# Kernel optimization log

Hardware: AMD Instinct MI355X
Metric: run time of the kernel (lower is better)

The kernel has to match this reference:

```python
import jax, jax.numpy as jnp
import numpy as np

N = 100000   # nodes
E = 1600000  # edges (before self-loops)
H = 128      # in_channels == hidden_channels
G = 64       # graphs in batch


def setup_inputs() -> dict:
    key = jax.random.key(0)
    ks = jax.random.split(key, 12)
    s = 1.0 / np.sqrt(H)
    inp = {
        "x": jax.random.normal(ks[0], (N, H), jnp.float32),
        "edge_weight": jax.random.uniform(ks[1], (E,), jnp.float32),
        "edge_index": jax.random.randint(ks[2], (2, E), 0, N, dtype=jnp.int64),
        "batch": jnp.sort(jax.random.randint(ks[3], (N,), 0, G, dtype=jnp.int64)),
        "W1": jax.random.uniform(ks[4], (H, H), jnp.float32, -s, s),
        "b1": jnp.zeros((H,), jnp.float32),
        "W2": jax.random.uniform(ks[5], (H, H), jnp.float32, -s, s),
        "b2": jnp.zeros((H,), jnp.float32),
        "W3": jax.random.uniform(ks[6], (H, H), jnp.float32, -s, s),
        "b3": jnp.zeros((H,), jnp.float32),
        "lin_w": jax.random.uniform(ks[7], (H, 1), jnp.float32, -s, s),
        "lin_b": jax.random.uniform(ks[8], (1,), jnp.float32, -s, s),
    }
    return inp


def reference(x, edge_weight, W1, b1, W2, b2, W3, b3, lin_w, lin_b, edge_index, batch):
    # PyG GCNConv with add_self_loops=True, symmetric normalization.
    loops = jnp.arange(N, dtype=edge_index.dtype)
    row = jnp.concatenate([edge_index[0], loops])  # source
    col = jnp.concatenate([edge_index[1], loops])  # target
    ew = jnp.concatenate([edge_weight, jnp.ones((N,), edge_weight.dtype)])

    deg = jax.ops.segment_sum(ew, col, num_segments=N)          # in-degree (weighted)
    safe = jnp.where(deg > 0, deg, 1.0)
    dinv = jnp.where(deg > 0, jax.lax.rsqrt(safe), 0.0)
    norm = dinv[row] * ew * dinv[col]                            # [E+N]

    def conv(h, W, b):
        h = h @ W                                                # [N,H] dense transform
        msg = h[row] * norm[:, None]                             # gather + scale
        return jax.ops.segment_sum(msg, col, num_segments=N) + b # scatter-add

    h = jax.nn.relu(conv(x, W1, b1))
    h = jax.nn.relu(conv(h, W2, b2))
    h = jax.nn.relu(conv(h, W3, b3))

    # global_mean_pool over graph ids
    sums = jax.ops.segment_sum(h, batch, num_segments=G)         # [G,H]
    cnts = jax.ops.segment_sum(jnp.ones((N,), h.dtype), batch, num_segments=G)
    pooled = sums / jnp.maximum(cnts, 1.0)[:, None]
    # dropout is identity at inference
    return pooled @ lin_w + lin_b                                # [G,1]
```

## Files before the change

kernel.cpp:

```cpp
#include <hip/hip_runtime.h>
#include <stdint.h>

#define N_NODES 100000
#define N_EDGES 1600000
#define HDIM    128
#define G_GRAPHS 64
#define NTOT (N_EDGES + N_NODES)
#define PSLOTS 64
#define NSTRIPS (N_NODES / 16)
#define NTB 512
#define NDB ((N_EDGES + 2047) / 2048)
#define BSH 9
#define NBK ((N_NODES + 511) / 512)
#define MAXBKT 10240

static_assert(N_NODES % 16 == 0, "tile/agg");
static_assert(N_NODES < (1 << 17), "src fits 17 bits");

typedef __attribute__((ext_vector_type(8))) short bf16x8;
typedef __attribute__((ext_vector_type(4))) float f32x4;
typedef __attribute__((ext_vector_type(2))) float f32x2;

__device__ __forceinline__ uint32_t f2bf(float x) {
    uint32_t b = __float_as_uint(x);
    return (b + 0x7FFFu + ((b >> 16) & 1u)) >> 16;
}
__device__ __forceinline__ uint32_t pack2(float lo, float hi) {
    return f2bf(lo) | (f2bf(hi) << 16);
}

#define FXSCALE 1099511627776.0f

__global__ void k_wswz(const float* __restrict__ Wb, const float* __restrict__ Wc,
                       uint16_t* __restrict__ dst) {
    int gi = blockIdx.x * 256 + threadIdx.x;
    int w = gi >> 14, idx = gi & 16383;
    const float* src = (w == 0) ? Wb : Wc;
    int k = idx >> 7, n = idx & 127;
    int kc = k >> 5, kq = (k >> 3) & 3, j = k & 7;
    int nt = n >> 4, nl = n & 15;
    dst[w * 16384 + (((kc * 8 + nt) * 64) + kq * 16 + nl) * 8 + j] = (uint16_t)f2bf(src[idx]);
}

__device__ __forceinline__ bf16x8 load_row_f32(const float* p) {
    float4 a = ((const float4*)p)[0];
    float4 b = ((const float4*)p)[1];
    union { uint32_t u[4]; bf16x8 v; } c;
    c.u[0] = pack2(a.x, a.y); c.u[1] = pack2(a.z, a.w);
    c.u[2] = pack2(b.x, b.y); c.u[3] = pack2(b.z, b.w);
    return c.v;
}

__device__ __forceinline__ void transform_body_l1(int tb, int nTB, int tid,
                                                  const float* __restrict__ hin,
                                                  const float* __restrict__ Wg,
                                                  uint32_t* __restrict__ t,
                                                  uint16_t* Wf) {
    for (int idx = tid; idx < 16384; idx += 256) {
        int k = idx >> 7, n = idx & 127;
        int kc = k >> 5, kq = (k >> 3) & 3, j = k & 7;
        int nt = n >> 4, nl = n & 15;
        Wf[(((kc * 8 + nt) * 64) + kq * 16 + nl) * 8 + j] = (uint16_t)f2bf(Wg[idx]);
    }
    __syncthreads();
    const bf16x8* Wfrag = (const bf16x8*)Wf;
    int lane = tid & 63;
    int quad = lane >> 4;
    int mrow = lane & 15;
    int gwave = tb * 4 + (tid >> 6);
    int nwaves = nTB * 4;
    for (int strip = gwave; strip < NSTRIPS; strip += nwaves) {
        const float* hrow = hin + ((size_t)(strip * 16 + mrow)) * 128 + quad * 8;
        bf16x8 A0 = load_row_f32(hrow);
        bf16x8 A1 = load_row_f32(hrow + 32);
        bf16x8 A2 = load_row_f32(hrow + 64);
        bf16x8 A3 = load_row_f32(hrow + 96);
        f32x4 acc[8];
#pragma unroll
        for (int nt = 0; nt < 8; nt++) {
            f32x4 a = {0.f, 0.f, 0.f, 0.f};
            a = __builtin_amdgcn_mfma_f32_16x16x32_bf16(A0, Wfrag[(0 * 8 + nt) * 64 + lane], a, 0, 0, 0);
            a = __builtin_amdgcn_mfma_f32_16x16x32_bf16(A1, Wfrag[(1 * 8 + nt) * 64 + lane], a, 0, 0, 0);
            a = __builtin_amdgcn_mfma_f32_16x16x32_bf16(A2, Wfrag[(2 * 8 + nt) * 64 + lane], a, 0, 0, 0);
            a = __builtin_amdgcn_mfma_f32_16x16x32_bf16(A3, Wfrag[(3 * 8 + nt) * 64 + lane], a, 0, 0, 0);
            acc[nt] = a;
        }
#pragma unroll
        for (int nt = 0; nt < 8; nt++) {
#pragma unroll
            for (int r = 0; r < 4; r++) {
                float v = acc[nt][r];
                float nb = __shfl_xor(v, 1);
                int s16 = __builtin_amdgcn_cvt_pk_fp8_f32(v, nb, 0, false);
                int hi  = __shfl_xor(s16, 2);
                if (!(lane & 3)) {
                    int orow = strip * 16 + quad * 4 + r;
                    int oc = (nt * 16 + mrow) >> 2;
                    t[(size_t)orow * 32 + oc] = (uint32_t)(s16 & 0xffff) | ((uint32_t)hi << 16);
                }
            }
        }
    }
}

__global__ __launch_bounds__(256) void k_tr_count(
        const int* __restrict__ ei, const float* __restrict__ x,
        const float* __restrict__ Wg, uint32_t* __restrict__ t,
        int* __restrict__ partials) {
    __shared__ uint16_t Wf[16384];
    int bi = blockIdx.x;
    int q5 = bi / 5, r5 = bi % 5;
    int tq = q5 * 2 + r5;
    bool isT = (r5 < 2) && (tq < NTB);
    int tid = threadIdx.x;
    if (isT) {
        transform_body_l1(tq, NTB, tid, x, Wg, t, Wf);
    } else {
        int nTbef = q5 * 2 + (r5 < 2 ? r5 : 2);
        if (nTbef > NTB) nTbef = NTB;
        int db = bi - nTbef;
        int* hist = (int*)Wf;
        for (int i = tid; i < NBK; i += 256) hist[i] = 0;
        __syncthreads();
        int e0 = db * 2048 + tid;
#pragma unroll
        for (int k = 0; k < 8; k++) {
            int e = e0 + k * 256;
            if (e < N_EDGES) atomicAdd(&hist[ei[N_EDGES + e] >> BSH], 1);
        }
        __syncthreads();
        for (int i = tid; i < NBK; i += 256) partials[i * NDB + db] = hist[i];
    }
}

__global__ void k_bscan(const int* __restrict__ partials, int* __restrict__ blockBase,
                        int* __restrict__ totals) {
    int b = blockIdx.x, tid = threadIdx.x;
    int v[4]; int s = 0;
#pragma unroll
    for (int j = 0; j < 4; j++) {
        int i = tid * 4 + j;
        v[j] = (i < NDB) ? partials[b * NDB + i] : 0;
        s += v[j];
    }
    __shared__ int sm[256];
    sm[tid] = s; __syncthreads();
    for (int off = 1; off < 256; off <<= 1) {
        int u = 0; if (tid >= off) u = sm[tid - off];
        __syncthreads(); sm[tid] += u; __syncthreads();
    }
    int run = sm[tid] - s;
#pragma unroll
    for (int j = 0; j < 4; j++) {
        int i = tid * 4 + j;
        if (i < NDB) blockBase[b * NDB + i] = run;
        run += v[j];
    }
    if (tid == 255) totals[b] = sm[255];
}

__global__ void k_starts(const int* __restrict__ totals, int* __restrict__ bstart) {
    int tid = threadIdx.x;
    int v = (tid < NBK) ? totals[tid] : 0;
    __shared__ int sm[256];
    sm[tid] = v; __syncthreads();
    for (int off = 1; off < 256; off <<= 1) {
        int u = 0; if (tid >= off) u = sm[tid - off];
        __syncthreads(); sm[tid] += u; __syncthreads();
    }
    if (tid < NBK) bstart[tid] = sm[tid] - v;
    if (tid == 255) bstart[NBK] = sm[255];
}

__global__ __launch_bounds__(256) void k_scatter(
        const int* __restrict__ ei, const float* __restrict__ ew,
        const int* __restrict__ blockBase, const int* __restrict__ bstart,
        uint2* __restrict__ recs) {
    __shared__ int hist[NBK];
    __shared__ int basesh[NBK];
    int tid = threadIdx.x, db = blockIdx.x;
    for (int i = tid; i < NBK; i += 256) {
        hist[i] = 0;
        basesh[i] = bstart[i] + blockBase[i * NDB + db];
    }
    __syncthreads();
    int e0 = db * 2048 + tid;
#pragma unroll
    for (int k = 0; k < 8; k++) {
        int e = e0 + k * 256;
        if (e < N_EDGES) {
            int src = ei[e];
            int dst = ei[N_EDGES + e];
            float w = ew[e];
            int bkt = dst >> BSH;
            int r = atomicAdd(&hist[bkt], 1);
            recs[basesh[bkt] + r] =
                make_uint2((uint32_t)src | ((uint32_t)(dst & 511) << 17),
                           __float_as_uint(w));
        }
    }
}

__global__ __launch_bounds__(256) void k_build(
        const uint2* __restrict__ recs, const int* __restrict__ bstart,
        int* __restrict__ cnt, float* __restrict__ dinv, int* __restrict__ offs,
        int2* __restrict__ csr) {
    __shared__ unsigned long long acc[512];
    __shared__ uint16_t rk[MAXBKT];
    __shared__ int loff[512];
    __shared__ int sm[256];
    int b = blockIdx.x, tid = threadIdx.x;
    int e0 = bstart[b], ne = bstart[b + 1] - e0;
    for (int i = tid; i < 512; i += 256) acc[i] = 0ULL;
    __syncthreads();
    for (int j = tid; j < ne; j += 256) {
        uint2 rc = recs[e0 + j];
        int dl = (rc.x >> 17) & 511;
        float w = __uint_as_float(rc.y);
        unsigned long long pk = (1ULL << 48) | (unsigned long long)(w * FXSCALE);
        unsigned long long old = atomicAdd(&acc[dl], pk);
        rk[j] = (uint16_t)(old >> 48);
    }
    __syncthreads();
    int nb0 = b << BSH;
    int nreal = N_NODES - nb0; if (nreal > 512) nreal = 512;
    int i0 = tid * 2, i1 = tid * 2 + 1;
    int c0 = (i0 < nreal) ? (int)(acc[i0] >> 48) + 1 : 0;
    int c1 = (i1 < nreal) ? (int)(acc[i1] >> 48) + 1 : 0;
    sm[tid] = c0 + c1;
    __syncthreads();
    for (int off = 1; off < 256; off <<= 1) {
        int u = 0; if (tid >= off) u = sm[tid - off];
        __syncthreads(); sm[tid] += u; __syncthreads();
    }
    int run = e0 + nb0 + (sm[tid] - (c0 + c1));
    loff[i0] = run;
    loff[i1] = run + c0;
    if (i0 < nreal) {
        unsigned long long pk = acc[i0];
        int c = (int)(pk >> 48);
        float deg = (float)(pk & ((1ULL << 48) - 1)) * (1.0f / FXSCALE);
        cnt[nb0 + i0] = c;
        offs[nb0 + i0] = run;
        dinv[nb0 + i0] = 1.0f / sqrtf(deg + 1.0f);
        csr[run + c] = make_int2(nb0 + i0, __float_as_int(1.0f));
    }
    if (i1 < nreal) {
        unsigned long long pk = acc[i1];
        int c = (int)(pk >> 48);
        float deg = (float)(pk & ((1ULL << 48) - 1)) * (1.0f / FXSCALE);
        cnt[nb0 + i1] = c;
        offs[nb0 + i1] = run + c0;
        dinv[nb0 + i1] = 1.0f / sqrtf(deg + 1.0f);
        csr[run + c0 + c] = make_int2(nb0 + i1, __float_as_int(1.0f));
    }
    __syncthreads();
    for (int j = tid; j < ne; j += 256) {
        uint2 rc = recs[e0 + j];
        int dl = (rc.x >> 17) & 511;
        int src = rc.x & 0x1ffff;
        csr[loff[dl] + rk[j]] = make_int2(src, (int)rc.y);
    }
}

__global__ void k_norm(int2* __restrict__ csr, const float* __restrict__ dinv) {
    int p = blockIdx.x * 256 + threadIdx.x;
    if (p < NTOT) {
        int2 c = csr[p];
        csr[p].y = __float_as_int(__int_as_float(c.y) * dinv[c.x]);
    }
}

__device__ __forceinline__ void fetch8(const char* __restrict__ tb, int g4, int lq8,
                                       int base, uint32_t osrc, float wsrc,
                                       uint2 (&va)[8], float (&wf)[8]) {
#pragma unroll
    for (int k = 0; k < 8; k++) {
        int o  = __builtin_amdgcn_ds_bpermute(g4 + base + 4 * k, (int)osrc);
        int wb = __builtin_amdgcn_ds_bpermute(g4 + base + 4 * k, __float_as_int(wsrc));
        wf[k] = __uint_as_float((uint32_t)wb);
        va[k] = *(const uint2*)(tb + (uint32_t)(o + lq8));
    }
}

__device__ __forceinline__ void acc8(const uint2 (&va)[8], const float (&wf)[8],
                                     f32x2& p0, f32x2& p1, f32x2& p2, f32x2& p3) {
#pragma unroll
    for (int k = 0; k < 8; k++) {
        f32x2 lo0 = __builtin_amdgcn_cvt_pk_f32_fp8((int)va[k].x, false);
        f32x2 hi0 = __builtin_amdgcn_cvt_pk_f32_fp8((int)va[k].x, true);
        f32x2 lo1 = __builtin_amdgcn_cvt_pk_f32_fp8((int)va[k].y, false);
        f32x2 hi1 = __builtin_amdgcn_cvt_pk_f32_fp8((int)va[k].y, true);
        f32x2 wp = { wf[k], wf[k] };
        p0 += wp * lo0; p1 += wp * hi0; p2 += wp * lo1; p3 += wp * hi1;
    }
}

__device__ __forceinline__ void aggregate_node(const char* __restrict__ tb,
        const int2* __restrict__ csr, int beg, int num, int ql, int g4, int lq8,
        f32x2& p0, f32x2& p1, f32x2& p2, f32x2& p3) {
    int2 m0 = make_int2(0, 0), m1 = make_int2(0, 0);
    if (ql < num) m0 = csr[beg + ql];
    if (ql + 16 < num) m1 = csr[beg + 16 + ql];
    uint32_t o0 = (uint32_t)m0.x << 7;
    uint32_t o1 = (uint32_t)m1.x << 7;
    float w0 = __int_as_float(m0.y), w1 = __int_as_float(m1.y);
    bool c1 = num > 8, c2 = num > 16, c3 = num > 24;
    uint2 va[8], vb[8], vc[8], vd[8];
    float wa[8], wb[8], wc[8], wd[8];
    fetch8(tb, g4, lq8, 0, o0, w0, va, wa);
    if (c1) fetch8(tb, g4, lq8, 32, o0, w0, vb, wb);
    acc8(va, wa, p0, p1, p2, p3);
    if (c2) fetch8(tb, g4, lq8, 0, o1, w1, vc, wc);
    if (c1) acc8(vb, wb, p0, p1, p2, p3);
    if (c3) fetch8(tb, g4, lq8, 32, o1, w1, vd, wd);
    if (c2) acc8(vc, wc, p0, p1, p2, p3);
    if (c3) acc8(vd, wd, p0, p1, p2, p3);
    for (int base = 32; base < num; base += 16) {
        int2 mm = make_int2(0, 0);
        if (base + ql < num) mm = csr[beg + base + ql];
        uint32_t oo = (uint32_t)mm.x << 7;
        float mws = __int_as_float(mm.y);
        bool h = base + 8 < num;
        fetch8(tb, g4, lq8, 0, oo, mws, va, wa);
        if (h) fetch8(tb, g4, lq8, 32, oo, mws, vb, wb);
        acc8(va, wa, p0, p1, p2, p3);
        if (h) acc8(vb, wb, p0, p1, p2, p3);
    }
}

__device__ __forceinline__ f32x2 relu2(f32x2 p, float dn, f32x2 b) {
    f32x2 r;
    r.x = fmaxf(p.x * dn + b.x, 0.f);
    r.y = fmaxf(p.y * dn + b.y, 0.f);
    return r;
}

__global__ __launch_bounds__(256) void k_agg_tr(
        const uint32_t* __restrict__ tin, const int* __restrict__ offs,
        const int* __restrict__ cnt, const int2* __restrict__ csr,
        const float* __restrict__ dinv, const float* __restrict__ bias,
        const bf16x8* __restrict__ Wfrag, uint32_t* __restrict__ tout) {
    __shared__ uint32_t ht[16 * 16 * 4];
    int tid = threadIdx.x;
    int lane = tid & 63;
    int ql = lane & 15;
    int grp = lane & 48;
    int g4 = grp << 2, lq8 = ql << 3;
    int row = (tid >> 6) * 4 + (lane >> 4);
    int node = blockIdx.x * 16 + row;
    int beg = offs[node];
    int num = cnt[node] + 1;
    float dn = dinv[node];
    f32x2 p0 = {0.f, 0.f}, p1 = {0.f, 0.f}, p2 = {0.f, 0.f}, p3 = {0.f, 0.f};
    aggregate_node((const char*)tin, csr, beg, num, ql, g4, lq8, p0, p1, p2, p3);
    const f32x2* bp = (const f32x2*)bias;
    p0 = relu2(p0, dn, bp[ql * 4 + 0]);
    p1 = relu2(p1, dn, bp[ql * 4 + 1]);
    p2 = relu2(p2, dn, bp[ql * 4 + 2]);
    p3 = relu2(p3, dn, bp[ql * 4 + 3]);
    {
        int slot = (ql + row) & 15;
        uint32_t* dst = &ht[(row * 16 + slot) * 4];
        dst[0] = pack2(p0.x, p0.y);
        dst[1] = pack2(p1.x, p1.y);
        dst[2] = pack2(p2.x, p2.y);
        dst[3] = pack2(p3.x, p3.y);
    }
    __syncthreads();
    int quad = lane >> 4;
    int m = lane & 15;
    int wid = tid >> 6;
    bf16x8 A[4];
#pragma unroll
    for (int c = 0; c < 4; c++) {
        int sl = (c * 4 + quad + m) & 15;
        A[c] = *(const bf16x8*)&ht[(m * 16 + sl) * 4];
    }
    int strip = blockIdx.x;
#pragma unroll
    for (int u = 0; u < 2; u++) {
        int nt = wid * 2 + u;
        f32x4 a = {0.f, 0.f, 0.f, 0.f};
        a = __builtin_amdgcn_mfma_f32_16x16x32_bf16(A[0], Wfrag[(0 * 8 + nt) * 64 + lane], a, 0, 0, 0);
        a = __builtin_amdgcn_mfma_f32_16x16x32_bf16(A[1], Wfrag[(1 * 8 + nt) * 64 + lane], a, 0, 0, 0);
        a = __builtin_amdgcn_mfma_f32_16x16x32_bf16(A[2], Wfrag[(2 * 8 + nt) * 64 + lane], a, 0, 0, 0);
        a = __builtin_amdgcn_mfma_f32_16x16x32_bf16(A[3], Wfrag[(3 * 8 + nt) * 64 + lane], a, 0, 0, 0);
#pragma unroll
        for (int r = 0; r < 4; r++) {
            float v = a[r];
            float nb = __shfl_xor(v, 1);
            int s16 = __builtin_amdgcn_cvt_pk_fp8_f32(v, nb, 0, false);
            int hi  = __shfl_xor(s16, 2);
            if (!(lane & 3)) {
                int orow = strip * 16 + quad * 4 + r;
                int oc = (nt * 16 + m) >> 2;
                tout[(size_t)orow * 32 + oc] = (uint32_t)(s16 & 0xffff) | ((uint32_t)hi << 16);
            }
        }
    }
}

__global__ void k_agg_pool(const uint32_t* __restrict__ t, const int* __restrict__ offs,
                           const int* __restrict__ cnt, const int2* __restrict__ csr,
                           const float* __restrict__ dinv, const float* __restrict__ bias,
                           const float* __restrict__ lw, const int* __restrict__ batch,
                           float* __restrict__ pp) {
    int tid = threadIdx.x;
    int lane = tid & 63;
    int ql = lane & 15;
    int grp = lane & 48;
    int g4 = grp << 2, lq8 = ql << 3;
    int node = blockIdx.x * 16 + (tid >> 6) * 4 + (lane >> 4);
    int beg = offs[node];
    int num = cnt[node] + 1;
    float dn = dinv[node];
    f32x2 p0 = {0.f, 0.f}, p1 = {0.f, 0.f}, p2 = {0.f, 0.f}, p3 = {0.f, 0.f};
    aggregate_node((const char*)t, csr, beg, num, ql, g4, lq8, p0, p1, p2, p3);
    const f32x2* bp = (const f32x2*)bias;
    p0 = relu2(p0, dn, bp[ql * 4 + 0]);
    p1 = relu2(p1, dn, bp[ql * 4 + 1]);
    p2 = relu2(p2, dn, bp[ql * 4 + 2]);
    p3 = relu2(p3, dn, bp[ql * 4 + 3]);
    const f32x2* wp2 = (const f32x2*)lw;
    f32x2 q0 = wp2[ql * 4 + 0], q1 = wp2[ql * 4 + 1];
    f32x2 q2 = wp2[ql * 4 + 2], q3 = wp2[ql * 4 + 3];
    float d = p0.x * q0.x + p0.y * q0.y + p1.x * q1.x + p1.y * q1.y
            + p2.x * q2.x + p2.y * q2.y + p3.x * q3.x + p3.y * q3.y;
    for (int off = 8; off; off >>= 1) d += __shfl_down(d, off);
    if (ql == 0)
        atomicAdd(&pp[(blockIdx.x & (PSLOTS - 1)) * G_GRAPHS + batch[node]], d);
}

__global__ void k_final(const float* __restrict__ pp, const int* __restrict__ batch,
                        const float* __restrict__ lb, float* __restrict__ out) {
    int g = threadIdx.x;
    float s = 0.f;
#pragma unroll
    for (int k = 0; k < PSLOTS; k++) s += pp[k * G_GRAPHS + g];
    int lo = 0, hi = N_NODES;
    while (lo < hi) { int m = (lo + hi) >> 1; if (batch[m] < g) lo = m + 1; else hi = m; }
    int beg = lo;
    hi = N_NODES;
    while (lo < hi) { int m = (lo + hi) >> 1; if (batch[m] < g + 1) lo = m + 1; else hi = m; }
    float c = fmaxf((float)(lo - beg), 1.0f);
    out[g] = s / c + lb[0];
}

extern "C" void kernel_launch(void* const* d_in, const int* in_sizes, int n_in,
                              void* d_out, int out_size, void* d_ws, size_t ws_size,
                              hipStream_t stream) {
    const float* x   = (const float*)d_in[0];
    const float* ew  = (const float*)d_in[1];
    const int*   ei  = (const int*)d_in[2];
    const int*   bat = (const int*)d_in[3];
    const float* W1  = (const float*)d_in[4];
    const float* b1  = (const float*)d_in[5];
    const float* W2  = (const float*)d_in[6];
    const float* b2  = (const float*)d_in[7];
    const float* W3  = (const float*)d_in[8];
    const float* b3  = (const float*)d_in[9];
    const float* lw  = (const float*)d_in[10];
    const float* lb  = (const float*)d_in[11];
    float* out = (float*)d_out;

    char* w = (char*)d_ws;
    size_t o = 0;
    auto carve = [&](size_t bytes) -> void* {
        void* p = w + o;
        o = (o + bytes + 255) & ~(size_t)255;
        return p;
    };
    float*    pp     = (float*)carve((size_t)PSLOTS * G_GRAPHS * 4);
    int*      parts  = (int*)  carve((size_t)NBK * NDB * 4);
    int*      bbase  = (int*)  carve((size_t)NBK * NDB * 4);
    int*      totals = (int*)  carve((size_t)NBK * 4);
    int*      bstart = (int*)  carve((size_t)(NBK + 1) * 4);
    uint2*    recs   = (uint2*)carve((size_t)N_EDGES * 8);
    int*      cnt    = (int*)  carve((size_t)N_NODES * 4);
    float*    dinv   = (float*)carve((size_t)N_NODES * 4);
    int*      offs   = (int*)  carve((size_t)N_NODES * 4);
    int2*     csr    = (int2*) carve((size_t)NTOT * 8);
    uint32_t* tA     = (uint32_t*)carve((size_t)N_NODES * 128);
    uint32_t* tB     = (uint32_t*)carve((size_t)N_NODES * 128);
    uint16_t* wsz    = (uint16_t*)carve((size_t)2 * 16384 * 2);
    (void)ws_size; (void)in_sizes; (void)n_in; (void)out_size;

    hipMemsetAsync(pp, 0, (size_t)PSLOTS * G_GRAPHS * 4, stream);

    k_wswz<<<128, 256, 0, stream>>>(W2, W3, wsz);
    k_tr_count<<<NTB + NDB, 256, 0, stream>>>(ei, x, W1, tA, parts);
    k_bscan<<<NBK, 256, 0, stream>>>(parts, bbase, totals);
    k_starts<<<1, 256, 0, stream>>>(totals, bstart);
    k_scatter<<<NDB, 256, 0, stream>>>(ei, ew, bbase, bstart, recs);
    k_build<<<NBK, 256, 0, stream>>>(recs, bstart, cnt, dinv, offs, csr);
    k_norm<<<(NTOT + 255) / 256, 256, 0, stream>>>(csr, dinv);

    k_agg_tr<<<NSTRIPS, 256, 0, stream>>>(tA, offs, cnt, csr, dinv, b1,
                                          (const bf16x8*)wsz, tB);
    k_agg_tr<<<NSTRIPS, 256, 0, stream>>>(tB, offs, cnt, csr, dinv, b2,
                                          (const bf16x8*)(wsz + 16384), tA);
    k_agg_pool<<<NSTRIPS, 256, 0, stream>>>(tA, offs, cnt, csr, dinv, b3, lw, bat, pp);

    k_final<<<1, G_GRAPHS, 0, stream>>>(pp, bat, lb, out);
}
```

Measured before the change: 343.2 us.

## Pre-swizzle W1 globally, use persistent aggregation grid, swap bpermute for ds_swizzle

W1 is now pre-swizzled to bf16 once in k_wswz, so transform blocks read MFMA fragments from global memory instead of each block converting W1 into shared memory. NTB is doubled and the block interleave ratio changed. The aggregation kernels move to a grid-stride loop over a fixed AGRID of 2048 blocks, which adds a second barrier per strip. The first 32 neighbours are now broadcast with ds_swizzle instead of ds_bpermute, and all four fetch batches are issued before accumulation to raise memory-level parallelism, at the cost of higher register pressure.

```diff
diff --git a/kernel.cpp b/kernel.cpp
--- a/kernel.cpp
+++ b/kernel.cpp
@@ -8,11 +8,12 @@
 #define NTOT (N_EDGES + N_NODES)
 #define PSLOTS 64
 #define NSTRIPS (N_NODES / 16)
-#define NTB 512
+#define NTB 1024
 #define NDB ((N_EDGES + 2047) / 2048)
 #define BSH 9
 #define NBK ((N_NODES + 511) / 512)
 #define MAXBKT 10240
+#define AGRID 2048
 
 static_assert(N_NODES % 16 == 0, "tile/agg");
 static_assert(N_NODES < (1 << 17), "src fits 17 bits");
@@ -31,11 +32,11 @@
 
 #define FXSCALE 1099511627776.0f
 
-__global__ void k_wswz(const float* __restrict__ Wb, const float* __restrict__ Wc,
-                       uint16_t* __restrict__ dst) {
+__global__ void k_wswz(const float* __restrict__ Wa, const float* __restrict__ Wb,
+                       const float* __restrict__ Wc, uint16_t* __restrict__ dst) {
     int gi = blockIdx.x * 256 + threadIdx.x;
     int w = gi >> 14, idx = gi & 16383;
-    const float* src = (w == 0) ? Wb : Wc;
+    const float* src = (w == 0) ? Wa : (w == 1) ? Wb : Wc;
     int k = idx >> 7, n = idx & 127;
     int kc = k >> 5, kq = (k >> 3) & 3, j = k & 7;
     int nt = n >> 4, nl = n & 15;
@@ -53,17 +54,8 @@
 
 __device__ __forceinline__ void transform_body_l1(int tb, int nTB, int tid,
                                                   const float* __restrict__ hin,
-                                                  const float* __restrict__ Wg,
-                                                  uint32_t* __restrict__ t,
-                                                  uint16_t* Wf) {
-    for (int idx = tid; idx < 16384; idx += 256) {
-        int k = idx >> 7, n = idx & 127;
-        int kc = k >> 5, kq = (k >> 3) & 3, j = k & 7;
-        int nt = n >> 4, nl = n & 15;
-        Wf[(((kc * 8 + nt) * 64) + kq * 16 + nl) * 8 + j] = (uint16_t)f2bf(Wg[idx]);
-    }
-    __syncthreads();
-    const bf16x8* Wfrag = (const bf16x8*)Wf;
+                                                  const bf16x8* __restrict__ Wfrag,
+                                                  uint32_t* __restrict__ t) {
     int lane = tid & 63;
     int quad = lane >> 4;
     int mrow = lane & 15;
@@ -105,21 +97,20 @@
 
 __global__ __launch_bounds__(256) void k_tr_count(
         const int* __restrict__ ei, const float* __restrict__ x,
-        const float* __restrict__ Wg, uint32_t* __restrict__ t,
+        const bf16x8* __restrict__ Wfrag, uint32_t* __restrict__ t,
         int* __restrict__ partials) {
-    __shared__ uint16_t Wf[16384];
+    __shared__ int hist[NBK];
     int bi = blockIdx.x;
-    int q5 = bi / 5, r5 = bi % 5;
-    int tq = q5 * 2 + r5;
-    bool isT = (r5 < 2) && (tq < NTB);
+    int q7 = bi / 7, r7 = bi % 7;
+    int tq = q7 * 4 + r7;
+    bool isT = (r7 < 4) && (tq < NTB);
     int tid = threadIdx.x;
     if (isT) {
-        transform_body_l1(tq, NTB, tid, x, Wg, t, Wf);
+        transform_body_l1(tq, NTB, tid, x, Wfrag, t);
     } else {
-        int nTbef = q5 * 2 + (r5 < 2 ? r5 : 2);
+        int nTbef = q7 * 4 + (r7 < 4 ? r7 : 4);
         if (nTbef > NTB) nTbef = NTB;
         int db = bi - nTbef;
-        int* hist = (int*)Wf;
         for (int i = tid; i < NBK; i += 256) hist[i] = 0;
         __syncthreads();
         int e0 = db * 2048 + tid;
@@ -271,9 +262,24 @@
     }
 }
 
-__device__ __forceinline__ void fetch8(const char* __restrict__ tb, int g4, int lq8,
-                                       int base, uint32_t osrc, float wsrc,
-                                       uint2 (&va)[8], float (&wf)[8]) {
+#define FETCH1(j, osrc, wsrc, vv, ww) { \
+    int o_ = __builtin_amdgcn_ds_swizzle((int)(osrc), (((j) << 5) | 0x10)); \
+    int w_ = __builtin_amdgcn_ds_swizzle((int)(wsrc), (((j) << 5) | 0x10)); \
+    ww = __uint_as_float((uint32_t)w_); \
+    vv = *(const uint2*)(tb + (uint32_t)o_ + lq8); }
+#define FETCH8S(J, osrc, wsrc, va, wa) \
+    FETCH1((J) + 0, osrc, wsrc, va[0], wa[0]) \
+    FETCH1((J) + 1, osrc, wsrc, va[1], wa[1]) \
+    FETCH1((J) + 2, osrc, wsrc, va[2], wa[2]) \
+    FETCH1((J) + 3, osrc, wsrc, va[3], wa[3]) \
+    FETCH1((J) + 4, osrc, wsrc, va[4], wa[4]) \
+    FETCH1((J) + 5, osrc, wsrc, va[5], wa[5]) \
+    FETCH1((J) + 6, osrc, wsrc, va[6], wa[6]) \
+    FETCH1((J) + 7, osrc, wsrc, va[7], wa[7])
+
+__device__ __forceinline__ void fetch8b(const char* __restrict__ tb, int g4, int lq8,
+                                        int base, uint32_t osrc, float wsrc,
+                                        uint2 (&va)[8], float (&wf)[8]) {
 #pragma unroll
     for (int k = 0; k < 8; k++) {
         int o  = __builtin_amdgcn_ds_bpermute(g4 + base + 4 * k, (int)osrc);
@@ -297,35 +303,37 @@
 }
 
 __device__ __forceinline__ void aggregate_node(const char* __restrict__ tb,
-        const int2* __restrict__ csr, int beg, int num, int ql, int g4, int lq8,
+        const int2* __restrict__ csr, int beg, int num, int ql, int lane, int lq8,
         f32x2& p0, f32x2& p1, f32x2& p2, f32x2& p3) {
     int2 m0 = make_int2(0, 0), m1 = make_int2(0, 0);
     if (ql < num) m0 = csr[beg + ql];
     if (ql + 16 < num) m1 = csr[beg + 16 + ql];
     uint32_t o0 = (uint32_t)m0.x << 7;
     uint32_t o1 = (uint32_t)m1.x << 7;
-    float w0 = __int_as_float(m0.y), w1 = __int_as_float(m1.y);
     bool c1 = num > 8, c2 = num > 16, c3 = num > 24;
     uint2 va[8], vb[8], vc[8], vd[8];
     float wa[8], wb[8], wc[8], wd[8];
-    fetch8(tb, g4, lq8, 0, o0, w0, va, wa);
-    if (c1) fetch8(tb, g4, lq8, 32, o0, w0, vb, wb);
+    FETCH8S(0, o0, m0.y, va, wa)
+    if (c1) { FETCH8S(8, o0, m0.y, vb, wb) }
+    if (c2) { FETCH8S(0, o1, m1.y, vc, wc) }
+    if (c3) { FETCH8S(8, o1, m1.y, vd, wd) }
     acc8(va, wa, p0, p1, p2, p3);
-    if (c2) fetch8(tb, g4, lq8, 0, o1, w1, vc, wc);
     if (c1) acc8(vb, wb, p0, p1, p2, p3);
-    if (c3) fetch8(tb, g4, lq8, 32, o1, w1, vd, wd);
     if (c2) acc8(vc, wc, p0, p1, p2, p3);
     if (c3) acc8(vd, wd, p0, p1, p2, p3);
-    for (int base = 32; base < num; base += 16) {
-        int2 mm = make_int2(0, 0);
-        if (base + ql < num) mm = csr[beg + base + ql];
-        uint32_t oo = (uint32_t)mm.x << 7;
-        float mws = __int_as_float(mm.y);
-        bool h = base + 8 < num;
-        fetch8(tb, g4, lq8, 0, oo, mws, va, wa);
-        if (h) fetch8(tb, g4, lq8, 32, oo, mws, vb, wb);
-        acc8(va, wa, p0, p1, p2, p3);
-        if (h) acc8(vb, wb, p0, p1, p2, p3);
+    if (num > 32) {
+        int g4 = (lane & 48) << 2;
+        for (int base = 32; base < num; base += 16) {
+            int2 mm = make_int2(0, 0);
+            if (base + ql < num) mm = csr[beg + base + ql];
+            uint32_t oo = (uint32_t)mm.x << 7;
+            float mws = __int_as_float(mm.y);
+            bool h = base + 8 < num;
+            fetch8b(tb, g4, lq8, 0, oo, mws, va, wa);
+            if (h) fetch8b(tb, g4, lq8, 32, oo, mws, vb, wb);
+            acc8(va, wa, p0, p1, p2, p3);
+            if (h) acc8(vb, wb, p0, p1, p2, p3);
+        }
     }
 }
 
@@ -345,91 +353,94 @@
     int tid = threadIdx.x;
     int lane = tid & 63;
     int ql = lane & 15;
-    int grp = lane & 48;
-    int g4 = grp << 2, lq8 = ql << 3;
+    int lq8 = ql << 3;
     int row = (tid >> 6) * 4 + (lane >> 4);
-    int node = blockIdx.x * 16 + row;
-    int beg = offs[node];
-    int num = cnt[node] + 1;
-    float dn = dinv[node];
-    f32x2 p0 = {0.f, 0.f}, p1 = {0.f, 0.f}, p2 = {0.f, 0.f}, p3 = {0.f, 0.f};
-    aggregate_node((const char*)tin, csr, beg, num, ql, g4, lq8, p0, p1, p2, p3);
-    const f32x2* bp = (const f32x2*)bias;
-    p0 = relu2(p0, dn, bp[ql * 4 + 0]);
-    p1 = relu2(p1, dn, bp[ql * 4 + 1]);
-    p2 = relu2(p2, dn, bp[ql * 4 + 2]);
-    p3 = relu2(p3, dn, bp[ql * 4 + 3]);
-    {
-        int slot = (ql + row) & 15;
-        uint32_t* dst = &ht[(row * 16 + slot) * 4];
-        dst[0] = pack2(p0.x, p0.y);
-        dst[1] = pack2(p1.x, p1.y);
-        dst[2] = pack2(p2.x, p2.y);
-        dst[3] = pack2(p3.x, p3.y);
-    }
-    __syncthreads();
     int quad = lane >> 4;
     int m = lane & 15;
     int wid = tid >> 6;
-    bf16x8 A[4];
-#pragma unroll
-    for (int c = 0; c < 4; c++) {
-        int sl = (c * 4 + quad + m) & 15;
-        A[c] = *(const bf16x8*)&ht[(m * 16 + sl) * 4];
-    }
-    int strip = blockIdx.x;
-#pragma unroll
-    for (int u = 0; u < 2; u++) {
-        int nt = wid * 2 + u;
-        f32x4 a = {0.f, 0.f, 0.f, 0.f};
-        a = __builtin_amdgcn_mfma_f32_16x16x32_bf16(A[0], Wfrag[(0 * 8 + nt) * 64 + lane], a, 0, 0, 0);
-        a = __builtin_amdgcn_mfma_f32_16x16x32_bf16(A[1], Wfrag[(1 * 8 + nt) * 64 + lane], a, 0, 0, 0);
-        a = __builtin_amdgcn_mfma_f32_16x16x32_bf16(A[2], Wfrag[(2 * 8 + nt) * 64 + lane], a, 0, 0, 0);
-        a = __builtin_amdgcn_mfma_f32_16x16x32_bf16(A[3], Wfrag[(3 * 8 + nt) * 64 + lane], a, 0, 0, 0);
-#pragma unroll
-        for (int r = 0; r < 4; r++) {
-            float v = a[r];
-            float nb = __shfl_xor(v, 1);
-            int s16 = __builtin_amdgcn_cvt_pk_fp8_f32(v, nb, 0, false);
-            int hi  = __shfl_xor(s16, 2);
-            if (!(lane & 3)) {
-                int orow = strip * 16 + quad * 4 + r;
-                int oc = (nt * 16 + m) >> 2;
-                tout[(size_t)orow * 32 + oc] = (uint32_t)(s16 & 0xffff) | ((uint32_t)hi << 16);
+    for (int strip = blockIdx.x; strip < NSTRIPS; strip += AGRID) {
+        int node = strip * 16 + row;
+        int beg = offs[node];
+        int num = cnt[node] + 1;
+        float dn = dinv[node];
+        f32x2 p0 = {0.f, 0.f}, p1 = {0.f, 0.f}, p2 = {0.f, 0.f}, p3 = {0.f, 0.f};
+        aggregate_node((const char*)tin, csr, beg, num, ql, lane, lq8, p0, p1, p2, p3);
+        const f32x2* bp = (const f32x2*)bias;
+        p0 = relu2(p0, dn, bp[ql * 4 + 0]);
+        p1 = relu2(p1, dn, bp[ql * 4 + 1]);
+        p2 = relu2(p2, dn, bp[ql * 4 + 2]);
+        p3 = relu2(p3, dn, bp[ql * 4 + 3]);
+        {
+            int slot = (ql + row) & 15;
+            uint32_t* dst = &ht[(row * 16 + slot) * 4];
+            dst[0] = pack2(p0.x, p0.y);
+            dst[1] = pack2(p1.x, p1.y);
+            dst[2] = pack2(p2.x, p2.y);
+            dst[3] = pack2(p3.x, p3.y);
+        }
+        __syncthreads();
+        bf16x8 A[4];
+#pragma unroll
+        for (int c = 0; c < 4; c++) {
+            int sl = (c * 4 + quad + m) & 15;
+            A[c] = *(const bf16x8*)&ht[(m * 16 + sl) * 4];
+        }
+        __syncthreads();
+#pragma unroll
+        for (int u = 0; u < 2; u++) {
+            int nt = wid * 2 + u;
+            f32x4 a = {0.f, 0.f, 0.f, 0.f};
+            a = __builtin_amdgcn_mfma_f32_16x16x32_bf16(A[0], Wfrag[(0 * 8 + nt) * 64 + lane], a, 0, 0, 0);
+            a = __builtin_amdgcn_mfma_f32_16x16x32_bf16(A[1], Wfrag[(1 * 8 + nt) * 64 + lane], a, 0, 0, 0);
+            a = __builtin_amdgcn_mfma_f32_16x16x32_bf16(A[2], Wfrag[(2 * 8 + nt) * 64 + lane], a, 0, 0, 0);
+            a = __builtin_amdgcn_mfma_f32_16x16x32_bf16(A[3], Wfrag[(3 * 8 + nt) * 64 + lane], a, 0, 0, 0);
+#pragma unroll
+            for (int r = 0; r < 4; r++) {
+                float v = a[r];
+                float nb = __shfl_xor(v, 1);
+                int s16 = __builtin_amdgcn_cvt_pk_fp8_f32(v, nb, 0, false);
+                int hi  = __shfl_xor(s16, 2);
+                if (!(lane & 3)) {
+                    int orow = strip * 16 + quad * 4 + r;
+                    int oc = (nt * 16 + m) >> 2;
+                    tout[(size_t)orow * 32 + oc] = (uint32_t)(s16 & 0xffff) | ((uint32_t)hi << 16);
+                }
             }
         }
     }
 }
 
-__global__ void k_agg_pool(const uint32_t* __restrict__ t, const int* __restrict__ offs,
-                           const int* __restrict__ cnt, const int2* __restrict__ csr,
-                           const float* __restrict__ dinv, const float* __restrict__ bias,
-                           const float* __restrict__ lw, const int* __restrict__ batch,
-                           float* __restrict__ pp) {
+__global__ __launch_bounds__(256) void k_agg_pool(
+        const uint32_t* __restrict__ t, const int* __restrict__ offs,
+        const int* __restrict__ cnt, const int2* __restrict__ csr,
+        const float* __restrict__ dinv, const float* __restrict__ bias,
+        const float* __restrict__ lw, const int* __restrict__ batch,
+        float* __restrict__ pp) {
     int tid = threadIdx.x;
     int lane = tid & 63;
     int ql = lane & 15;
-    int grp = lane & 48;
-    int g4 = grp << 2, lq8 = ql << 3;
-    int node = blockIdx.x * 16 + (tid >> 6) * 4 + (lane >> 4);
-    int beg = offs[node];
-    int num = cnt[node] + 1;
-    float dn = dinv[node];
-    f32x2 p0 = {0.f, 0.f}, p1 = {0.f, 0.f}, p2 = {0.f, 0.f}, p3 = {0.f, 0.f};
-    aggregate_node((const char*)t, csr, beg, num, ql, g4, lq8, p0, p1, p2, p3);
-    const f32x2* bp = (const f32x2*)bias;
-    p0 = relu2(p0, dn, bp[ql * 4 + 0]);
-    p1 = relu2(p1, dn, bp[ql * 4 + 1]);
-    p2 = relu2(p2, dn, bp[ql * 4 + 2]);
-    p3 = relu2(p3, dn, bp[ql * 4 + 3]);
-    const f32x2* wp2 = (const f32x2*)lw;
-    f32x2 q0 = wp2[ql * 4 + 0], q1 = wp2[ql * 4 + 1];
-    f32x2 q2 = wp2[ql * 4 + 2], q3 = wp2[ql * 4 + 3];
-    float d = p0.x * q0.x + p0.y * q0.y + p1.x * q1.x + p1.y * q1.y
-            + p2.x * q2.x + p2.y * q2.y + p3.x * q3.x + p3.y * q3.y;
-    for (int off = 8; off; off >>= 1) d += __shfl_down(d, off);
-    if (ql == 0)
-        atomicAdd(&pp[(blockIdx.x & (PSLOTS - 1)) * G_GRAPHS + batch[node]], d);
+    int lq8 = ql << 3;
+    for (int strip = blockIdx.x; strip < NSTRIPS; strip += AGRID) {
+        int node = strip * 16 + (tid >> 6) * 4 + (lane >> 4);
+        int beg = offs[node];
+        int num = cnt[node] + 1;
+        float dn = dinv[node];
+        f32x2 p0 = {0.f, 0.f}, p1 = {0.f, 0.f}, p2 = {0.f, 0.f}, p3 = {0.f, 0.f};
+        aggregate_node((const char*)t, csr, beg, num, ql, lane, lq8, p0, p1, p2, p3);
+        const f32x2* bp = (const f32x2*)bias;
+        p0 = relu2(p0, dn, bp[ql * 4 + 0]);
+        p1 = relu2(p1, dn, bp[ql * 4 + 1]);
+        p2 = relu2(p2, dn, bp[ql * 4 + 2]);
+        p3 = relu2(p3, dn, bp[ql * 4 + 3]);
+        const f32x2* wp2 = (const f32x2*)lw;
+        f32x2 q0 = wp2[ql * 4 + 0], q1 = wp2[ql * 4 + 1];
+        f32x2 q2 = wp2[ql * 4 + 2], q3 = wp2[ql * 4 + 3];
+        float d = p0.x * q0.x + p0.y * q0.y + p1.x * q1.x + p1.y * q1.y
+                + p2.x * q2.x + p2.y * q2.y + p3.x * q3.x + p3.y * q3.y;
+        for (int off = 8; off; off >>= 1) d += __shfl_down(d, off);
+        if (ql == 0)
+            atomicAdd(&pp[(strip & (PSLOTS - 1)) * G_GRAPHS + batch[node]], d);
+    }
 }
 
 __global__ void k_final(const float* __restrict__ pp, const int* __restrict__ batch,
@@ -483,24 +494,24 @@
     int2*     csr    = (int2*) carve((size_t)NTOT * 8);
     uint32_t* tA     = (uint32_t*)carve((size_t)N_NODES * 128);
     uint32_t* tB     = (uint32_t*)carve((size_t)N_NODES * 128);
-    uint16_t* wsz    = (uint16_t*)carve((size_t)2 * 16384 * 2);
+    uint16_t* wsz    = (uint16_t*)carve((size_t)3 * 16384 * 2);
     (void)ws_size; (void)in_sizes; (void)n_in; (void)out_size;
 
     hipMemsetAsync(pp, 0, (size_t)PSLOTS * G_GRAPHS * 4, stream);
 
-    k_wswz<<<128, 256, 0, stream>>>(W2, W3, wsz);
-    k_tr_count<<<NTB + NDB, 256, 0, stream>>>(ei, x, W1, tA, parts);
+    k_wswz<<<192, 256, 0, stream>>>(W1, W2, W3, wsz);
+    k_tr_count<<<NTB + NDB, 256, 0, stream>>>(ei, x, (const bf16x8*)wsz, tA, parts);
     k_bscan<<<NBK, 256, 0, stream>>>(parts, bbase, totals);
     k_starts<<<1, 256, 0, stream>>>(totals, bstart);
     k_scatter<<<NDB, 256, 0, stream>>>(ei, ew, bbase, bstart, recs);
     k_build<<<NBK, 256, 0, stream>>>(recs, bstart, cnt, dinv, offs, csr);
     k_norm<<<(NTOT + 255) / 256, 256, 0, stream>>>(csr, dinv);
 
-    k_agg_tr<<<NSTRIPS, 256, 0, stream>>>(tA, offs, cnt, csr, dinv, b1,
-                                          (const bf16x8*)wsz, tB);
-    k_agg_tr<<<NSTRIPS, 256, 0, stream>>>(tB, offs, cnt, csr, dinv, b2,
-                                          (const bf16x8*)(wsz + 16384), tA);
-    k_agg_pool<<<NSTRIPS, 256, 0, stream>>>(tA, offs, cnt, csr, dinv, b3, lw, bat, pp);
+    k_agg_tr<<<AGRID, 256, 0, stream>>>(tA, offs, cnt, csr, dinv, b1,
+                                        (const bf16x8*)(wsz + 16384), tB);
+    k_agg_tr<<<AGRID, 256, 0, stream>>>(tB, offs, cnt, csr, dinv, b2,
+                                        (const bf16x8*)(wsz + 2 * 16384), tA);
+    k_agg_pool<<<AGRID, 256, 0, stream>>>(tA, offs, cnt, csr, dinv, b3, lw, bat, pp);
 
     k_final<<<1, G_GRAPHS, 0, stream>>>(pp, bat, lb, out);
 }
```

Measured after the change: 360.4 us. 5.0% more time.
